# Kernel tuning notes

Measured on AMD Instinct MI355X. Metric: run time of the kernel, lower is better.

## Reference

```python
import jax, jax.numpy as jnp
import numpy as np

B, N, IN, E, H, F = 64, 256, 128, 256, 8, 1024


def setup_inputs() -> dict:
    key = jax.random.key(0)
    ks = jax.random.split(key, 16)
    x = jax.random.normal(ks[0], (B, N, IN), jnp.float32)
    adj = (jax.random.uniform(ks[1], (B, N, N)) < 0.1).astype(jnp.float32)
    adj = jnp.maximum(adj, adj.transpose(0, 2, 1))  # symmetric 0/1 adjacency
    mask = jax.random.randint(ks[2], (B, N), 0, 2).astype(jnp.float32)
    dist = jax.random.normal(ks[3], (B, N, N), jnp.float32)

    def lin(k, i, o):
        return (jax.random.normal(k, (i, o), jnp.float32) / np.sqrt(i)).astype(jnp.float32)

    return dict(
        x=x, adj=adj, mask=mask, dist=dist,
        W1=lin(ks[4], IN, E), b1=jnp.zeros((E,), jnp.float32),
        W2=lin(ks[5], E, E), b2=jnp.zeros((E,), jnp.float32),
        W3=lin(ks[6], E, E), b3=jnp.zeros((E,), jnp.float32),
        ln1_g=jnp.ones((E,), jnp.float32), ln1_b=jnp.zeros((E,), jnp.float32),
        Wq=lin(ks[7], E, H * E), Wk=lin(ks[8], E, H * E), Wv=lin(ks[9], E, H * E),
        Wo=lin(ks[10], H * E, E), bo=jnp.zeros((E,), jnp.float32),
        ln2_g=jnp.ones((E,), jnp.float32), ln2_b=jnp.zeros((E,), jnp.float32),
        Wf1=lin(ks[11], E, F), bf1=jnp.zeros((F,), jnp.float32),
        Wf2=lin(ks[12], F, E), bf2=jnp.zeros((E,), jnp.float32),
    )


def _layernorm(x, g, b):
    m = x.mean(-1, keepdims=True)
    v = ((x - m) ** 2).mean(-1, keepdims=True)
    return (x - m) * jax.lax.rsqrt(v + 1e-5) * g + b


def reference(x, adj, mask, dist, W1, b1, W2, b2, W3, b3, ln1_g, ln1_b,
              Wq, Wk, Wv, Wo, bo, ln2_g, ln2_b, Wf1, bf1, Wf2, bf2):
    # --- DenseGCNConv normalization (add self-loops, sym-normalize) ---
    eye = jnp.eye(N, dtype=adj.dtype)
    A = adj * (1.0 - eye) + eye                      # fill_diag(adj, 1)
    dis = jax.lax.rsqrt(jnp.clip(A.sum(-1), 1.0, None))
    An = dis[:, :, None] * A * dis[:, None, :]       # D^-1/2 A D^-1/2, [B,N,N]
    m3 = mask[:, :, None]

    def gcn(h, W, b):
        return (jnp.einsum('bij,bjf->bif', An, h @ W) + b) * m3

    g1 = jax.nn.relu(gcn(x, W1, b1))
    g2 = jax.nn.relu(gcn(g1, W2, b2))
    g3 = jax.nn.relu(gcn(g2, W3, b3))
    gcn_res = g1 + g2 + g3

    # --- masked MHA with distance bias (head dim = E per head) ---
    h = _layernorm(gcn_res, ln1_g, ln1_b)
    mh = mask[:, None, :, None]                      # [B,1,N,1]
    q = (h @ Wq).reshape(B, N, H, E).transpose(0, 2, 1, 3) * mh
    k = (h @ Wk).reshape(B, N, H, E).transpose(0, 2, 1, 3) * mh
    v = (h @ Wv).reshape(B, N, H, E).transpose(0, 2, 1, 3) * mh
    a = jnp.einsum('bhne,bhme->bhnm', q * (E ** -0.5), k) + dist[:, None]
    am = (mask[:, :, None] * mask[:, None, :])[:, None]  # [B,1,N,N]
    a = jnp.where(am == 0, -1e9, a)
    a = jax.nn.softmax(a, axis=-1)
    a = jnp.where(am == 0, 0.0, a)
    y = jnp.einsum('bhnm,bhme->bhne', a, v).transpose(0, 2, 1, 3).reshape(B, N, H * E)
    y = (y @ Wo + bo) * m3
    att = gcn_res + y

    # --- FFN block ---
    f = _layernorm(att, ln2_g, ln2_b)
    f = (jax.nn.gelu(f @ Wf1 + bf1, approximate=False) @ Wf2 + bf2) * m3
    att = att + f
    return gcn_res + att
```

## Files before the change

kernel.cpp:

```cpp
#include <hip/hip_runtime.h>
#include <hip/hip_bf16.h>
#include <cmath>

#define BB 64
#define NNODES 256
#define INF_ 128
#define EE 256
#define HH 8
#define FFN 1024
#define BNROWS 16384

typedef __attribute__((ext_vector_type(8))) short short8;
typedef __attribute__((ext_vector_type(4))) float floatx4;
typedef __attribute__((ext_vector_type(4))) unsigned short ushort4v;

__device__ __forceinline__ float b2f(unsigned short u) {
  union { unsigned u32; float f; } w; w.u32 = ((unsigned)u) << 16; return w.f;
}
__device__ __forceinline__ unsigned short f2b(float f) {
  union { float f; unsigned u32; } w; w.f = f;
  unsigned r = w.u32 + 0x7FFFu + ((w.u32 >> 16) & 1u);
  return (unsigned short)(r >> 16);
}
__device__ __forceinline__ float gelu_f(float x) {
  const float z = 0.7978845608028654f * (x + 0.044715f * x * x * x);
  const float e = __expf(2.0f * z);
  const float th = (e - 1.0f) / (e + 1.0f);
  return 0.5f * x * (1.0f + th);
}

typedef const __attribute__((address_space(1))) void GV;
typedef __attribute__((address_space(3))) void LV;

__device__ __forceinline__ void gl_lds16(const unsigned short* g,
                                         unsigned short* l, int lane) {
#if __has_builtin(__builtin_amdgcn_global_load_lds)
  __builtin_amdgcn_global_load_lds((GV*)g, (LV*)l, 16, 0, 0);
#else
  *(short8*)(l + lane * 8) = *(const short8*)g;
#endif
}

__global__ void cvt_kernel(const float* __restrict__ src,
                           unsigned short* __restrict__ dst, int n)
{
  const int i = (blockIdx.x * 256 + threadIdx.x) * 4;
  if (i >= n) return;
  floatx4 v = *(const floatx4*)(src + i);
  ushort4v o;
  #pragma unroll
  for (int j = 0; j < 4; j++) o[j] = f2b(v[j]);
  *(ushort4v*)(dst + i) = o;
}

__global__ void tcvt_kernel(const float* __restrict__ src,
                            unsigned short* __restrict__ dst,
                            int R, int C)
{
  __shared__ float tile[32][33];
  const int c0 = blockIdx.x * 32, r0 = blockIdx.y * 32;
  const int tx = threadIdx.x, ty = threadIdx.y;
  #pragma unroll
  for (int i = ty; i < 32; i += 8)
    tile[i][tx] = src[(long long)(r0 + i) * C + c0 + tx];
  __syncthreads();
  #pragma unroll
  for (int i = ty; i < 32; i += 8)
    dst[(long long)(c0 + i) * R + r0 + tx] = f2b(tile[tx][i]);
}

__launch_bounds__(512, 4)
__global__ void gemm_kernel(const unsigned short* __restrict__ A, int lda,
                            long long sAo, long long sAi,
                            const unsigned short* __restrict__ Bm, int ldb,
                            long long sBo, long long sBi,
                            void* __restrict__ Cv, int ldc,
                            long long sCo, long long sCi,
                            int K, int zshift, int mode, int flag,
                            const float* __restrict__ aux1,
                            const float* __restrict__ mask,
                            float* __restrict__ gcn,
                            void* __restrict__ aux2)
{
  __shared__ __align__(16) unsigned short sA[16384];
  __shared__ __align__(16) unsigned short sB[16384];

  const int t = threadIdx.x;
  const int z = blockIdx.z;
  const int zi = z & ((1 << zshift) - 1);
  const int zb = z >> zshift;
  const int m0 = blockIdx.x * 128;
  const int n0 = blockIdx.y * 128;
  A  += zb * sAo + zi * sAi;
  Bm += zb * sBo + zi * sBi;
  const long long cbase = zb * sCo + zi * sCi;

  const int lane = t & 63;
  const int w = t >> 6;
  const int wm = w >> 2, wn = w & 3;
  const int lm = lane & 15, qd = lane >> 4;

  floatx4 acc[4][2] = {};

  const int sub = lane >> 4;
  const int qs  = lane & 15;
  const unsigned short* pA[4];
  const unsigned short* pB[4];
  #pragma unroll
  for (int i = 0; i < 4; i++) {
    const int d = w * 4 + i;
    const int r = d * 4 + sub;
    const int co = (qs ^ (r & 7)) * 8;
    pA[i] = A + (long long)(m0 + r) * lda + co;
    pB[i] = Bm + (long long)(n0 + r) * ldb + co;
  }

  for (int kk = 0; kk < K; kk += 128) {
    #pragma unroll
    for (int i = 0; i < 4; i++) {
      gl_lds16(pA[i] + kk, &sA[(w * 4 + i) * 512], lane);
      gl_lds16(pB[i] + kk, &sB[(w * 4 + i) * 512], lane);
    }
    __syncthreads();

    #pragma unroll
    for (int ks = 0; ks < 4; ks++) {
      short8 af[4], bg[2];
      const int q = ks * 4 + qd;
      #pragma unroll
      for (int mi = 0; mi < 4; mi++) {
        const int r = wm * 64 + mi * 16 + lm;
        af[mi] = *(const short8*)&sA[r * 128 + ((q ^ (r & 7)) * 8)];
      }
      #pragma unroll
      for (int ni = 0; ni < 2; ni++) {
        const int r = wn * 32 + ni * 16 + lm;
        bg[ni] = *(const short8*)&sB[r * 128 + ((q ^ (r & 7)) * 8)];
      }
      #pragma unroll
      for (int mi = 0; mi < 4; mi++)
        #pragma unroll
        for (int ni = 0; ni < 2; ni++)
          acc[mi][ni] = __builtin_amdgcn_mfma_f32_16x16x32_bf16(
              af[mi], bg[ni], acc[mi][ni], 0, 0, 0);
    }
    __syncthreads();
  }

  #pragma unroll
  for (int mi = 0; mi < 4; mi++) {
    const int row0 = m0 + wm * 64 + mi * 16 + qd * 4;
    #pragma unroll
    for (int ni = 0; ni < 2; ni++) {
      const int col = n0 + wn * 32 + ni * 16 + lm;
      floatx4 a = acc[mi][ni];
      if (mode == 0) {
        float* Cf = (float*)Cv;
        #pragma unroll
        for (int r = 0; r < 4; r++)
          Cf[cbase + (long long)(row0 + r) * ldc + col] = a[r];
      } else if (mode == 1) {
        unsigned short* Cb = (unsigned short*)Cv;
        #pragma unroll
        for (int r = 0; r < 4; r++)
          Cb[cbase + (long long)(row0 + r) * ldc + col] = f2b(a[r]);
      } else if (mode == 2) {
        float* Cf = (float*)Cv;
        #pragma unroll
        for (int r = 0; r < 4; r++)
          Cf[cbase + (long long)(row0 + r) * ldc + col] += a[r];
      } else if (mode == 3) {
        unsigned short* Cb = (unsigned short*)Cv;
        const float bv = aux1[col];
        #pragma unroll
        for (int r = 0; r < 4; r++)
          Cb[cbase + (long long)(row0 + r) * ldc + col] = f2b(gelu_f(a[r] + bv));
      } else if (mode == 5) {
        const int b = row0 >> 8, n = row0 & 255;
        ushort4v o;
        #pragma unroll
        for (int r = 0; r < 4; r++) o[r] = f2b(a[r]);
        *(ushort4v*)((unsigned short*)Cv + (long long)b * 65536 + col * 256 + n) = o;
      } else if (mode == 8) {
        float* Cf = (float*)Cv;
        const float* attf = (const float*)aux2;
        const float bv = aux1[col];
        #pragma unroll
        for (int r = 0; r < 4; r++) {
          const long long idx = (long long)(row0 + r) * 256 + col;
          Cf[idx] = gcn[idx] + attf[idx] + (a[r] + bv) * mask[row0 + r];
        }
      } else if (mode == 9) {
        const int token = zb * 256 + col;
        const float m = mask[token];
        ushort4v o; floatx4 g;
        #pragma unroll
        for (int r = 0; r < 4; r++) {
          const float v = fmaxf((a[r] + aux1[row0 + r]) * m, 0.f);
          o[r] = f2b(v); g[r] = v;
        }
        *(ushort4v*)((unsigned short*)Cv + (long long)token * 256 + row0) = o;
        float* gp = gcn + (long long)token * 256 + row0;
        if (flag) { floatx4 old = *(const floatx4*)gp; g += old; }
        *(floatx4*)gp = g;
      } else if (mode == 11) {
        if (col < 2048) {
          unsigned short* Cb = (unsigned short*)Cv;
          #pragma unroll
          for (int r = 0; r < 4; r++)
            Cb[(long long)(row0 + r) * 4096 + col] = f2b(a[r] * 0.0625f);
        } else if (col < 4096) {
          unsigned short* Cb = (unsigned short*)Cv;
          #pragma unroll
          for (int r = 0; r < 4; r++)
            Cb[(long long)(row0 + r) * 4096 + col] = f2b(a[r]);
        } else {
          const int z2 = (row0 >> 8) * 8 + ((col - 4096) >> 8);
          const int e = col & 255, n = row0 & 255;
          ushort4v o;
          #pragma unroll
          for (int r = 0; r < 4; r++) o[r] = f2b(a[r]);
          *(ushort4v*)((unsigned short*)aux2 + (long long)z2 * 65536 + e * 256 + n) = o;
        }
      } else {
        float* Cf = (float*)Cv;
        const float bv = aux1[col];
        #pragma unroll
        for (int r = 0; r < 4; r++) {
          const long long idx = (long long)(row0 + r) * 256 + col;
          Cf[idx] = gcn[idx] + (a[r] + bv) * mask[row0 + r];
        }
      }
    }
  }
}

__launch_bounds__(512, 2)
__global__ void attn_kernel(unsigned short* __restrict__ QKY,
                            const unsigned short* __restrict__ VT,
                            const float* __restrict__ dist,
                            const float* __restrict__ mask)
{
  __shared__ __align__(16) unsigned short sQ[8192];
  __shared__ __align__(16) unsigned short sKV[16384];
  __shared__ float redm[4][128];
  __shared__ float reds[4][128];

  const int mt = blockIdx.x;
  const int z  = blockIdx.y;
  const int b  = z >> 3, h = z & 7;
  const int t = threadIdx.x, lane = t & 63, w = t >> 6;
  const int wm = w >> 2, wn = w & 3;
  const int lm = lane & 15, qd = lane >> 4;
  const int m0 = mt * 128;

  unsigned short* Qbase = QKY + ((long long)(b * 256 + m0)) * 4096 + h * 256;
  const unsigned short* Kbase = QKY + ((long long)(b * 256)) * 4096 + 2048 + h * 256;
  const unsigned short* Vbase = VT + (long long)z * 65536;
  const float* maskb = mask + b * 256;
  const float* distb = dist + (long long)b * 65536;

  const int rin = lane >> 3;
  const int qs  = lane & 7;

  floatx4 S[4][4] = {};

  for (int c = 0; c < 4; c++) {
    const int e0 = c * 64;
    #pragma unroll
    for (int i = 0; i < 2; i++) {
      const int d = w * 2 + i;
      const int r = d * 8 + rin;
      gl_lds16(Qbase + (long long)r * 4096 + e0 + ((qs ^ (r & 7)) * 8),
               &sQ[d * 512], lane);
    }
    #pragma unroll
    for (int i = 0; i < 4; i++) {
      const int d = w * 4 + i;
      const int r = d * 8 + rin;
      gl_lds16(Kbase + (long long)r * 4096 + e0 + ((qs ^ (r & 7)) * 8),
               &sKV[d * 512], lane);
    }
    __syncthreads();
    #pragma unroll
    for (int ks = 0; ks < 2; ks++) {
      short8 af[4], bg[4];
      const int o = ks * 4 + qd;
      #pragma unroll
      for (int mi = 0; mi < 4; mi++) {
        const int r = wm * 64 + mi * 16 + lm;
        af[mi] = *(const short8*)&sQ[r * 64 + ((o ^ (r & 7)) * 8)];
      }
      #pragma unroll
      for (int ni = 0; ni < 4; ni++) {
        const int r = wn * 64 + ni * 16 + lm;
        bg[ni] = *(const short8*)&sKV[r * 64 + ((o ^ (r & 7)) * 8)];
      }
      #pragma unroll
      for (int mi = 0; mi < 4; mi++)
        #pragma unroll
        for (int ni = 0; ni < 4; ni++)
          S[mi][ni] = __builtin_amdgcn_mfma_f32_16x16x32_bf16(
              af[mi], bg[ni], S[mi][ni], 0, 0, 0);
    }
    __syncthreads();
  }

  float mk[4];
  #pragma unroll
  for (int ni = 0; ni < 4; ni++) mk[ni] = maskb[wn * 64 + ni * 16 + lm];

  float lred[4][4];
  #pragma unroll
  for (int mi = 0; mi < 4; mi++) {
    #pragma unroll
    for (int r = 0; r < 4; r++) {
      const int row = wm * 64 + mi * 16 + qd * 4 + r;
      const float mq = maskb[m0 + row];
      float mx = -3e38f;
      #pragma unroll
      for (int ni = 0; ni < 4; ni++) {
        const int col = wn * 64 + ni * 16 + lm;
        const float dv = distb[(long long)(m0 + row) * 256 + col];
        const float v = (mq != 0.f && mk[ni] != 0.f) ? (S[mi][ni][r] + dv) : -1e9f;
        S[mi][ni][r] = v;
        mx = fmaxf(mx, v);
      }
      lred[mi][r] = mx;
    }
  }
  #pragma unroll
  for (int off = 1; off < 16; off <<= 1)
    #pragma unroll
    for (int mi = 0; mi < 4; mi++)
      #pragma unroll
      for (int r = 0; r < 4; r++)
        lred[mi][r] = fmaxf(lred[mi][r], __shfl_xor(lred[mi][r], off));
  if (lm == 0)
    #pragma unroll
    for (int mi = 0; mi < 4; mi++)
      #pragma unroll
      for (int r = 0; r < 4; r++)
        redm[wn][wm * 64 + mi * 16 + qd * 4 + r] = lred[mi][r];
  __syncthreads();

  #pragma unroll
  for (int mi = 0; mi < 4; mi++) {
    #pragma unroll
    for (int r = 0; r < 4; r++) {
      const int row = wm * 64 + mi * 16 + qd * 4 + r;
      const float gmax = fmaxf(fmaxf(redm[0][row], redm[1][row]),
                               fmaxf(redm[2][row], redm[3][row]));
      float s = 0.f;
      #pragma unroll
      for (int ni = 0; ni < 4; ni++) {
        const float e = __expf(S[mi][ni][r] - gmax);
        S[mi][ni][r] = e;
        s += e;
      }
      lred[mi][r] = s;
    }
  }
  #pragma unroll
  for (int off = 1; off < 16; off <<= 1)
    #pragma unroll
    for (int mi = 0; mi < 4; mi++)
      #pragma unroll
      for (int r = 0; r < 4; r++)
        lred[mi][r] += __shfl_xor(lred[mi][r], off);
  if (lm == 0)
    #pragma unroll
    for (int mi = 0; mi < 4; mi++)
      #pragma unroll
      for (int r = 0; r < 4; r++)
        reds[wn][wm * 64 + mi * 16 + qd * 4 + r] = lred[mi][r];
  __syncthreads();

  #pragma unroll
  for (int mi = 0; mi < 4; mi++) {
    #pragma unroll
    for (int r = 0; r < 4; r++) {
      const int row = wm * 64 + mi * 16 + qd * 4 + r;
      const float gs = redm[0][row] * 0.f +
                       reds[0][row] + reds[1][row] + reds[2][row] + reds[3][row];
      const float inv = 1.0f / gs;
      #pragma unroll
      for (int ni = 0; ni < 4; ni++) S[mi][ni][r] *= inv;
    }
  }

  floatx4 Y[4][4] = {};
  for (int c = 0; c < 4; c++) {
    #pragma unroll
    for (int i = 0; i < 4; i++) {
      const int d = w * 4 + i;
      const int r = d * 8 + rin;
      gl_lds16(Vbase + (long long)r * 256 + c * 64 + ((qs ^ (r & 7)) * 8),
               &sKV[d * 512], lane);
    }
    if (wn == c) {
      #pragma unroll
      for (int mi = 0; mi < 4; mi++)
        #pragma unroll
        for (int r = 0; r < 4; r++) {
          const int row = wm * 64 + mi * 16 + qd * 4 + r;
          #pragma unroll
          for (int ni = 0; ni < 4; ni++) {
            const int kl = ni * 16 + lm;
            const int slot = (kl >> 3) ^ (row & 7);
            sQ[row * 64 + slot * 8 + (kl & 7)] = f2b(S[mi][ni][r]);
          }
        }
    }
    __syncthreads();
    #pragma unroll
    for (int ks = 0; ks < 2; ks++) {
      short8 af[4], bg[4];
      const int o = ks * 4 + qd;
      #pragma unroll
      for (int mi = 0; mi < 4; mi++) {
        const int r = wm * 64 + mi * 16 + lm;
        af[mi] = *(const short8*)&sQ[r * 64 + ((o ^ (r & 7)) * 8)];
      }
      #pragma unroll
      for (int ni = 0; ni < 4; ni++) {
        const int r = wn * 64 + ni * 16 + lm;
        bg[ni] = *(const short8*)&sKV[r * 64 + ((o ^ (r & 7)) * 8)];
      }
      #pragma unroll
      for (int mi = 0; mi < 4; mi++)
        #pragma unroll
        for (int ni = 0; ni < 4; ni++)
          Y[mi][ni] = __builtin_amdgcn_mfma_f32_16x16x32_bf16(
              af[mi], bg[ni], Y[mi][ni], 0, 0, 0);
    }
    __syncthreads();
  }

  #pragma unroll
  for (int mi = 0; mi < 4; mi++)
    #pragma unroll
    for (int ni = 0; ni < 4; ni++) {
      const int col = wn * 64 + ni * 16 + lm;
      #pragma unroll
      for (int r = 0; r < 4; r++) {
        const int row = wm * 64 + mi * 16 + qd * 4 + r;
        Qbase[(long long)row * 4096 + col] = f2b(Y[mi][ni][r]);
      }
    }
}

__global__ void deg_kernel(const float* __restrict__ adj,
                           float* __restrict__ dis)
{
  const int g = blockIdx.x * 4 + (threadIdx.x >> 6);
  const int lane = threadIdx.x & 63;
  const int i = g & 255;
  floatx4 v = *(const floatx4*)(adj + (long long)g * 256 + lane * 4);
  float s = 0.f;
  #pragma unroll
  for (int jj = 0; jj < 4; jj++) {
    const int j = lane * 4 + jj;
    s += (j == i) ? 1.0f : v[jj];
  }
  #pragma unroll
  for (int off = 32; off > 0; off >>= 1) s += __shfl_xor(s, off);
  if (lane == 0) dis[g] = 1.0f / sqrtf(fmaxf(s, 1.0f));
}

__global__ void an_kernel(const float* __restrict__ adj,
                          const float* __restrict__ dis,
                          unsigned short* __restrict__ An)
{
  const long long base = ((long long)blockIdx.x * 256 + threadIdx.x) * 4;
  const int rowg = (int)(base >> 8);
  const int i = rowg & 255;
  const int brow = rowg & ~255;
  const int j0 = (int)(base & 255);
  const float di = dis[rowg];
  floatx4 v = *(const floatx4*)(adj + base);
  ushort4v o;
  #pragma unroll
  for (int jj = 0; jj < 4; jj++) {
    const int j = j0 + jj;
    const float a = (j == i) ? 1.0f : v[jj];
    o[jj] = f2b(di * dis[brow + j] * a);
  }
  *(ushort4v*)(An + base) = o;
}

__global__ void ln_kernel(const float* __restrict__ X,
                          const float* __restrict__ gam,
                          const float* __restrict__ bet,
                          unsigned short* __restrict__ out)
{
  const int g = blockIdx.x * 4 + (threadIdx.x >> 6);
  const int lane = threadIdx.x & 63;
  floatx4 v = *(const floatx4*)(X + (long long)g * 256 + lane * 4);
  float s = v[0] + v[1] + v[2] + v[3];
  float sq = v[0]*v[0] + v[1]*v[1] + v[2]*v[2] + v[3]*v[3];
  #pragma unroll
  for (int off = 32; off > 0; off >>= 1) {
    s  += __shfl_xor(s, off);
    sq += __shfl_xor(sq, off);
  }
  const float mean = s * (1.0f / 256.0f);
  const float var = sq * (1.0f / 256.0f) - mean * mean;
  const float rs = 1.0f / sqrtf(var + 1e-5f);
  ushort4v o;
  #pragma unroll
  for (int jj = 0; jj < 4; jj++) {
    const int c = lane * 4 + jj;
    o[jj] = f2b((v[jj] - mean) * rs * gam[c] + bet[c]);
  }
  *(ushort4v*)(out + (long long)g * 256 + lane * 4) = o;
}

static inline void launch_gemm(hipStream_t st, int M, int N, int batch,
    const void* A, int lda, long long sAo, long long sAi,
    const void* B, int ldb, long long sBo, long long sBi,
    void* C, int ldc, long long sCo, long long sCi,
    int K, int zshift, int mode, int flag,
    const float* aux1, const float* mask, float* gcn, void* aux2)
{
  dim3 grid(M / 128, N / 128, batch), blk(512);
  gemm_kernel<<<grid, blk, 0, st>>>(
      (const unsigned short*)A, lda, sAo, sAi,
      (const unsigned short*)B, ldb, sBo, sBi,
      C, ldc, sCo, sCi, K, zshift, mode, flag, aux1, mask, gcn, aux2);
}

extern "C" void kernel_launch(void* const* d_in, const int* in_sizes, int n_in,
                              void* d_out, int out_size, void* d_ws, size_t ws_size,
                              hipStream_t stream)
{
  (void)in_sizes; (void)n_in; (void)out_size;
  const float* x    = (const float*)d_in[0];
  const float* adj  = (const float*)d_in[1];
  const float* mask = (const float*)d_in[2];
  const float* dist = (const float*)d_in[3];
  const float* W1   = (const float*)d_in[4];
  const float* b1   = (const float*)d_in[5];
  const float* W2   = (const float*)d_in[6];
  const float* b2   = (const float*)d_in[7];
  const float* W3   = (const float*)d_in[8];
  const float* b3   = (const float*)d_in[9];
  const float* ln1g = (const float*)d_in[10];
  const float* ln1b = (const float*)d_in[11];
  const float* Wq   = (const float*)d_in[12];
  const float* Wk   = (const float*)d_in[13];
  const float* Wv   = (const float*)d_in[14];
  const float* Wo   = (const float*)d_in[15];
  const float* bo   = (const float*)d_in[16];
  const float* ln2g = (const float*)d_in[17];
  const float* ln2b = (const float*)d_in[18];
  const float* Wf1  = (const float*)d_in[19];
  const float* bf1  = (const float*)d_in[20];
  const float* Wf2  = (const float*)d_in[21];
  const float* bf2  = (const float*)d_in[22];

  char* w = (char*)d_ws;
  auto alloc = [&](size_t sz) { void* p = (void*)w; w += sz; return p; };
  unsigned short* W1T   = (unsigned short*)alloc(65536);
  unsigned short* W2T   = (unsigned short*)alloc(131072);
  unsigned short* W3T   = (unsigned short*)alloc(131072);
  unsigned short* WQKVT = (unsigned short*)alloc(3145728);
  unsigned short* WOT   = (unsigned short*)alloc(1048576);
  unsigned short* WF1T  = (unsigned short*)alloc(524288);
  unsigned short* WF2T  = (unsigned short*)alloc(524288);
  unsigned short* XBF   = (unsigned short*)alloc(4194304);
  float*          GCN   = (float*)         alloc(16777216);
  float*          U     = (float*)         alloc(16777216);
  unsigned short* HBF   = (unsigned short*)alloc(8388608);
  float*          DIS   = (float*)         alloc(65536);
  char* scratch = (char*)alloc(201326592);
  if ((size_t)(w - (char*)d_ws) > ws_size) return;
  unsigned short* AN  = (unsigned short*)scratch;
  unsigned short* TT  = (unsigned short*)(scratch + 8388608);
  unsigned short* GBF = (unsigned short*)(scratch + 16777216);
  unsigned short* QKY = (unsigned short*)scratch;
  unsigned short* VT  = (unsigned short*)(scratch + 134217728);
  unsigned short* FFB = (unsigned short*)scratch;

  dim3 tb(32, 8);
  tcvt_kernel<<<dim3(8, 4),  tb, 0, stream>>>(W1,  W1T,  128,  256);
  tcvt_kernel<<<dim3(8, 8),  tb, 0, stream>>>(W2,  W2T,  256,  256);
  tcvt_kernel<<<dim3(8, 8),  tb, 0, stream>>>(W3,  W3T,  256,  256);
  tcvt_kernel<<<dim3(64, 8), tb, 0, stream>>>(Wq,  WQKVT,            256, 2048);
  tcvt_kernel<<<dim3(64, 8), tb, 0, stream>>>(Wk,  WQKVT + 2048*256, 256, 2048);
  tcvt_kernel<<<dim3(64, 8), tb, 0, stream>>>(Wv,  WQKVT + 4096*256, 256, 2048);
  tcvt_kernel<<<dim3(8, 64), tb, 0, stream>>>(Wo,  WOT,  2048,  256);
  tcvt_kernel<<<dim3(32, 8), tb, 0, stream>>>(Wf1, WF1T,  256, 1024);
  tcvt_kernel<<<dim3(8, 32), tb, 0, stream>>>(Wf2, WF2T, 1024,  256);
  cvt_kernel<<<2048, 256, 0, stream>>>(x, XBF, BNROWS * INF_);

  deg_kernel<<<4096, 256, 0, stream>>>(adj, DIS);
  an_kernel<<<4096, 256, 0, stream>>>(adj, DIS, AN);

  launch_gemm(stream, BNROWS, EE, 1, XBF, 128, 0,0, W1T, 128, 0,0,
              TT, 256, 0,0, 128, 0, 5, 0, nullptr, nullptr, nullptr, nullptr);
  launch_gemm(stream, 256, 256, BB, TT, 256, 65536,0, AN, 256, 65536,0,
              GBF, 256, 0,0, 256, 0, 9, 0, b1, mask, GCN, nullptr);
  launch_gemm(stream, BNROWS, EE, 1, GBF, 256, 0,0, W2T, 256, 0,0,
              TT, 256, 0,0, 256, 0, 5, 0, nullptr, nullptr, nullptr, nullptr);
  launch_gemm(stream, 256, 256, BB, TT, 256, 65536,0, AN, 256, 65536,0,
              GBF, 256, 0,0, 256, 0, 9, 1, b2, mask, GCN, nullptr);
  launch_gemm(stream, BNROWS, EE, 1, GBF, 256, 0,0, W3T, 256, 0,0,
              TT, 256, 0,0, 256, 0, 5, 0, nullptr, nullptr, nullptr, nullptr);
  launch_gemm(stream, 256, 256, BB, TT, 256, 65536,0, AN, 256, 65536,0,
              GBF, 256, 0,0, 256, 0, 9, 1, b3, mask, GCN, nullptr);

  ln_kernel<<<4096, 256, 0, stream>>>(GCN, ln1g, ln1b, HBF);

  launch_gemm(stream, BNROWS, 6144, 1, HBF, 256, 0,0, WQKVT, 256, 0,0,
              QKY, 4096, 0,0, 256, 0, 11, 0, nullptr, nullptr, nullptr, VT);
  attn_kernel<<<dim3(2, 512), 512, 0, stream>>>(QKY, VT, dist, mask);
  launch_gemm(stream, BNROWS, EE, 1, QKY, 4096, 0,0, WOT, 2048, 0,0,
              U, 256, 0,0, 2048, 0, 12, 0, bo, mask, GCN, nullptr);

  ln_kernel<<<4096, 256, 0, stream>>>(U, ln2g, ln2b, HBF);
  launch_gemm(stream, BNROWS, FFN, 1, HBF, 256, 0,0, WF1T, 256, 0,0,
              FFB, 1024, 0,0, 256, 0, 3, 0, bf1, nullptr, nullptr, nullptr);
  launch_gemm(stream, BNROWS, EE, 1, FFB, 1024, 0,0, WF2T, 1024, 0,0,
              d_out, 256, 0,0, 1024, 0, 8, 0, bf2, mask, GCN, U);
}
```

Before: 532.3 us.

## Merge weight packing launches, fuse degree/normalization, prefetch V, split QKV+attention by batch

Ten separate weight/input conversion launches become one pack_kernel that dispatches on block index. The degree and normalization kernels are fused into one per-batch kernel that keeps inverse-sqrt degrees in shared memory. In attention, the V chunk load is issued before the softmax and the next chunk is prefetched after each PV step, so loads overlap compute. The QKV GEMM and attention are split into two batch halves, which may improve cache locality at the cost of extra launches. The fused normalization kernel runs only 64 blocks, which may underuse the GPU.

```diff
diff --git a/kernel.cpp b/kernel.cpp
--- a/kernel.cpp
+++ b/kernel.cpp
@@ -41,25 +41,38 @@
 #endif
 }
 
-__global__ void cvt_kernel(const float* __restrict__ src,
-                           unsigned short* __restrict__ dst, int n)
-{
-  const int i = (blockIdx.x * 256 + threadIdx.x) * 4;
-  if (i >= n) return;
-  floatx4 v = *(const floatx4*)(src + i);
-  ushort4v o;
-  #pragma unroll
-  for (int j = 0; j < 4; j++) o[j] = f2b(v[j]);
-  *(ushort4v*)(dst + i) = o;
-}
-
-__global__ void tcvt_kernel(const float* __restrict__ src,
-                            unsigned short* __restrict__ dst,
-                            int R, int C)
+struct PackArgs {
+  const float* src[10];
+  unsigned short* dst[10];
+  int R[10], C[10];
+  int start[11];
+};
+
+__launch_bounds__(256)
+__global__ void pack_kernel(PackArgs a)
 {
   __shared__ float tile[32][33];
-  const int c0 = blockIdx.x * 32, r0 = blockIdx.y * 32;
-  const int tx = threadIdx.x, ty = threadIdx.y;
+  const int bid = blockIdx.x;
+  int j = 0;
+  while (bid >= a.start[j + 1]) j++;
+  const int lb = bid - a.start[j];
+  const float* src = a.src[j];
+  unsigned short* dst = a.dst[j];
+  const int R = a.R[j], C = a.C[j];
+
+  if (C == 0) {
+    const int i = (lb * 256 + threadIdx.x) * 4;
+    if (i >= R) return;
+    floatx4 v = *(const floatx4*)(src + i);
+    ushort4v o;
+    #pragma unroll
+    for (int k = 0; k < 4; k++) o[k] = f2b(v[k]);
+    *(ushort4v*)(dst + i) = o;
+    return;
+  }
+  const int tpr = C >> 5;
+  const int c0 = (lb % tpr) * 32, r0 = (lb / tpr) * 32;
+  const int tx = threadIdx.x & 31, ty = threadIdx.x >> 5;
   #pragma unroll
   for (int i = ty; i < 32; i += 8)
     tile[i][tx] = src[(long long)(r0 + i) * C + c0 + tx];
@@ -67,6 +80,43 @@
   #pragma unroll
   for (int i = ty; i < 32; i += 8)
     dst[(long long)(c0 + i) * R + r0 + tx] = f2b(tile[tx][i]);
+}
+
+__launch_bounds__(1024)
+__global__ void an_kernel(const float* __restrict__ adj,
+                          unsigned short* __restrict__ An)
+{
+  __shared__ float dis[256];
+  const int b = blockIdx.x;
+  const float* A = adj + (long long)b * 65536;
+  const int t = threadIdx.x;
+  const int row = t >> 2, seg = t & 3;
+  const float* p = A + row * 256 + seg * 64;
+  float s = 0.f;
+  for (int k = 0; k < 64; k += 4) {
+    floatx4 v = *(const floatx4*)(p + k);
+    #pragma unroll
+    for (int jj = 0; jj < 4; jj++) {
+      const int col = seg * 64 + k + jj;
+      s += (col == row) ? 1.0f : v[jj];
+    }
+  }
+  s += __shfl_xor(s, 1);
+  s += __shfl_xor(s, 2);
+  if (seg == 0) dis[row] = 1.0f / sqrtf(fmaxf(s, 1.0f));
+  __syncthreads();
+  const float di = dis[row];
+  unsigned short* dst = An + (long long)b * 65536 + row * 256 + seg * 64;
+  for (int k = 0; k < 64; k += 4) {
+    floatx4 v = *(const floatx4*)(p + k);
+    ushort4v o;
+    #pragma unroll
+    for (int jj = 0; jj < 4; jj++) {
+      const int col = seg * 64 + k + jj;
+      o[jj] = f2b(di * dis[col] * ((col == row) ? 1.0f : v[jj]));
+    }
+    *(ushort4v*)(dst + k) = o;
+  }
 }
 
 __launch_bounds__(512, 4)
@@ -239,7 +289,8 @@
 __global__ void attn_kernel(unsigned short* __restrict__ QKY,
                             const unsigned short* __restrict__ VT,
                             const float* __restrict__ dist,
-                            const float* __restrict__ mask)
+                            const float* __restrict__ mask,
+                            int b0)
 {
   __shared__ __align__(16) unsigned short sQ[8192];
   __shared__ __align__(16) unsigned short sKV[16384];
@@ -248,17 +299,18 @@
 
   const int mt = blockIdx.x;
   const int z  = blockIdx.y;
-  const int b  = z >> 3, h = z & 7;
+  const int bl = z >> 3, h = z & 7;
+  const int bg = b0 + bl;
   const int t = threadIdx.x, lane = t & 63, w = t >> 6;
   const int wm = w >> 2, wn = w & 3;
   const int lm = lane & 15, qd = lane >> 4;
   const int m0 = mt * 128;
 
-  unsigned short* Qbase = QKY + ((long long)(b * 256 + m0)) * 4096 + h * 256;
-  const unsigned short* Kbase = QKY + ((long long)(b * 256)) * 4096 + 2048 + h * 256;
+  unsigned short* Qbase = QKY + ((long long)(bl * 256 + m0)) * 4096 + h * 256;
+  const unsigned short* Kbase = QKY + ((long long)(bl * 256)) * 4096 + 2048 + h * 256;
   const unsigned short* Vbase = VT + (long long)z * 65536;
-  const float* maskb = mask + b * 256;
-  const float* distb = dist + (long long)b * 65536;
+  const float* maskb = mask + bg * 256;
+  const float* distb = dist + (long long)bg * 65536;
 
   const int rin = lane >> 3;
   const int qs  = lane & 7;
@@ -284,7 +336,7 @@
     __syncthreads();
     #pragma unroll
     for (int ks = 0; ks < 2; ks++) {
-      short8 af[4], bg[4];
+      short8 af[4], bg4[4];
       const int o = ks * 4 + qd;
       #pragma unroll
       for (int mi = 0; mi < 4; mi++) {
@@ -294,16 +346,24 @@
       #pragma unroll
       for (int ni = 0; ni < 4; ni++) {
         const int r = wn * 64 + ni * 16 + lm;
-        bg[ni] = *(const short8*)&sKV[r * 64 + ((o ^ (r & 7)) * 8)];
+        bg4[ni] = *(const short8*)&sKV[r * 64 + ((o ^ (r & 7)) * 8)];
       }
       #pragma unroll
       for (int mi = 0; mi < 4; mi++)
         #pragma unroll
         for (int ni = 0; ni < 4; ni++)
           S[mi][ni] = __builtin_amdgcn_mfma_f32_16x16x32_bf16(
-              af[mi], bg[ni], S[mi][ni], 0, 0, 0);
+              af[mi], bg4[ni], S[mi][ni], 0, 0, 0);
     }
     __syncthreads();
+  }
+
+  #pragma unroll
+  for (int i = 0; i < 4; i++) {
+    const int d = w * 4 + i;
+    const int r = d * 8 + rin;
+    gl_lds16(Vbase + (long long)r * 256 + ((qs ^ (r & 7)) * 8),
+             &sKV[d * 512], lane);
   }
 
   float mk[4];
@@ -381,8 +441,7 @@
     #pragma unroll
     for (int r = 0; r < 4; r++) {
       const int row = wm * 64 + mi * 16 + qd * 4 + r;
-      const float gs = redm[0][row] * 0.f +
-                       reds[0][row] + reds[1][row] + reds[2][row] + reds[3][row];
+      const float gs = reds[0][row] + reds[1][row] + reds[2][row] + reds[3][row];
       const float inv = 1.0f / gs;
       #pragma unroll
       for (int ni = 0; ni < 4; ni++) S[mi][ni][r] *= inv;
@@ -391,13 +450,6 @@
 
   floatx4 Y[4][4] = {};
   for (int c = 0; c < 4; c++) {
-    #pragma unroll
-    for (int i = 0; i < 4; i++) {
-      const int d = w * 4 + i;
-      const int r = d * 8 + rin;
-      gl_lds16(Vbase + (long long)r * 256 + c * 64 + ((qs ^ (r & 7)) * 8),
-               &sKV[d * 512], lane);
-    }
     if (wn == c) {
       #pragma unroll
       for (int mi = 0; mi < 4; mi++)
@@ -415,7 +467,7 @@
     __syncthreads();
     #pragma unroll
     for (int ks = 0; ks < 2; ks++) {
-      short8 af[4], bg[4];
+      short8 af[4], bg4[4];
       const int o = ks * 4 + qd;
       #pragma unroll
       for (int mi = 0; mi < 4; mi++) {
@@ -425,16 +477,25 @@
       #pragma unroll
       for (int ni = 0; ni < 4; ni++) {
         const int r = wn * 64 + ni * 16 + lm;
-        bg[ni] = *(const short8*)&sKV[r * 64 + ((o ^ (r & 7)) * 8)];
+        bg4[ni] = *(const short8*)&sKV[r * 64 + ((o ^ (r & 7)) * 8)];
       }
       #pragma unroll
       for (int mi = 0; mi < 4; mi++)
         #pragma unroll
         for (int ni = 0; ni < 4; ni++)
           Y[mi][ni] = __builtin_amdgcn_mfma_f32_16x16x32_bf16(
-              af[mi], bg[ni], Y[mi][ni], 0, 0, 0);
+              af[mi], bg4[ni], Y[mi][ni], 0, 0, 0);
     }
     __syncthreads();
+    if (c < 3) {
+      #pragma unroll
+      for (int i = 0; i < 4; i++) {
+        const int d = w * 4 + i;
+        const int r = d * 8 + rin;
+        gl_lds16(Vbase + (long long)r * 256 + (c + 1) * 64 + ((qs ^ (r & 7)) * 8),
+                 &sKV[d * 512], lane);
+      }
+    }
   }
 
   #pragma unroll
@@ -448,45 +509,6 @@
         Qbase[(long long)row * 4096 + col] = f2b(Y[mi][ni][r]);
       }
     }
-}
-
-__global__ void deg_kernel(const float* __restrict__ adj,
-                           float* __restrict__ dis)
-{
-  const int g = blockIdx.x * 4 + (threadIdx.x >> 6);
-  const int lane = threadIdx.x & 63;
-  const int i = g & 255;
-  floatx4 v = *(const floatx4*)(adj + (long long)g * 256 + lane * 4);
-  float s = 0.f;
-  #pragma unroll
-  for (int jj = 0; jj < 4; jj++) {
-    const int j = lane * 4 + jj;
-    s += (j == i) ? 1.0f : v[jj];
-  }
-  #pragma unroll
-  for (int off = 32; off > 0; off >>= 1) s += __shfl_xor(s, off);
-  if (lane == 0) dis[g] = 1.0f / sqrtf(fmaxf(s, 1.0f));
-}
-
-__global__ void an_kernel(const float* __restrict__ adj,
-                          const float* __restrict__ dis,
-                          unsigned short* __restrict__ An)
-{
-  const long long base = ((long long)blockIdx.x * 256 + threadIdx.x) * 4;
-  const int rowg = (int)(base >> 8);
-  const int i = rowg & 255;
-  const int brow = rowg & ~255;
-  const int j0 = (int)(base & 255);
-  const float di = dis[rowg];
-  floatx4 v = *(const floatx4*)(adj + base);
-  ushort4v o;
-  #pragma unroll
-  for (int jj = 0; jj < 4; jj++) {
-    const int j = j0 + jj;
-    const float a = (j == i) ? 1.0f : v[jj];
-    o[jj] = f2b(di * dis[brow + j] * a);
-  }
-  *(ushort4v*)(An + base) = o;
 }
 
 __global__ void ln_kernel(const float* __restrict__ X,
@@ -572,7 +594,6 @@
   float*          GCN   = (float*)         alloc(16777216);
   float*          U     = (float*)         alloc(16777216);
   unsigned short* HBF   = (unsigned short*)alloc(8388608);
-  float*          DIS   = (float*)         alloc(65536);
   char* scratch = (char*)alloc(201326592);
   if ((size_t)(w - (char*)d_ws) > ws_size) return;
   unsigned short* AN  = (unsigned short*)scratch;
@@ -582,20 +603,20 @@
   unsigned short* VT  = (unsigned short*)(scratch + 134217728);
   unsigned short* FFB = (unsigned short*)scratch;
 
-  dim3 tb(32, 8);
-  tcvt_kernel<<<dim3(8, 4),  tb, 0, stream>>>(W1,  W1T,  128,  256);
-  tcvt_kernel<<<dim3(8, 8),  tb, 0, stream>>>(W2,  W2T,  256,  256);
-  tcvt_kernel<<<dim3(8, 8),  tb, 0, stream>>>(W3,  W3T,  256,  256);
-  tcvt_kernel<<<dim3(64, 8), tb, 0, stream>>>(Wq,  WQKVT,            256, 2048);
-  tcvt_kernel<<<dim3(64, 8), tb, 0, stream>>>(Wk,  WQKVT + 2048*256, 256, 2048);
-  tcvt_kernel<<<dim3(64, 8), tb, 0, stream>>>(Wv,  WQKVT + 4096*256, 256, 2048);
-  tcvt_kernel<<<dim3(8, 64), tb, 0, stream>>>(Wo,  WOT,  2048,  256);
-  tcvt_kernel<<<dim3(32, 8), tb, 0, stream>>>(Wf1, WF1T,  256, 1024);
-  tcvt_kernel<<<dim3(8, 32), tb, 0, stream>>>(Wf2, WF2T, 1024,  256);
-  cvt_kernel<<<2048, 256, 0, stream>>>(x, XBF, BNROWS * INF_);
-
-  deg_kernel<<<4096, 256, 0, stream>>>(adj, DIS);
-  an_kernel<<<4096, 256, 0, stream>>>(adj, DIS, AN);
+  PackArgs pa;
+  const float* srcs[10] = {W1, W2, W3, Wq, Wk, Wv, Wo, Wf1, Wf2, x};
+  unsigned short* dsts[10] = {W1T, W2T, W3T, WQKVT, WQKVT + 2048*256,
+                              WQKVT + 4096*256, WOT, WF1T, WF2T, XBF};
+  const int Rs[10] = {128, 256, 256, 256, 256, 256, 2048, 256, 1024, BNROWS * INF_};
+  const int Cs[10] = {256, 256, 256, 2048, 2048, 2048, 256, 1024, 256, 0};
+  const int sts[11] = {0, 32, 96, 160, 672, 1184, 1696, 2208, 2464, 2720, 4768};
+  for (int j = 0; j < 10; j++) {
+    pa.src[j] = srcs[j]; pa.dst[j] = dsts[j]; pa.R[j] = Rs[j]; pa.C[j] = Cs[j];
+  }
+  for (int j = 0; j < 11; j++) pa.start[j] = sts[j];
+  pack_kernel<<<4768, 256, 0, stream>>>(pa);
+
+  an_kernel<<<64, 1024, 0, stream>>>(adj, AN);
 
   launch_gemm(stream, BNROWS, EE, 1, XBF, 128, 0,0, W1T, 128, 0,0,
               TT, 256, 0,0, 128, 0, 5, 0, nullptr, nullptr, nullptr, nullptr);
@@ -612,9 +633,14 @@
 
   ln_kernel<<<4096, 256, 0, stream>>>(GCN, ln1g, ln1b, HBF);
 
-  launch_gemm(stream, BNROWS, 6144, 1, HBF, 256, 0,0, WQKVT, 256, 0,0,
-              QKY, 4096, 0,0, 256, 0, 11, 0, nullptr, nullptr, nullptr, VT);
-  attn_kernel<<<dim3(2, 512), 512, 0, stream>>>(QKY, VT, dist, mask);
+  for (int g = 0; g < 2; g++) {
+    unsigned short* QKYg = QKY + (long long)g * 8192 * 4096;
+    unsigned short* VTg  = VT  + (long long)g * 256 * 65536;
+    launch_gemm(stream, 8192, 6144, 1, HBF + (long long)g * 8192 * 256, 256, 0,0,
+                WQKVT, 256, 0,0,
+                QKYg, 4096, 0,0, 256, 0, 11, 0, nullptr, nullptr, nullptr, VTg);
+    attn_kernel<<<dim3(2, 256), 512, 0, stream>>>(QKYg, VTg, dist, mask, g * 32);
+  }
   launch_gemm(stream, BNROWS, EE, 1, QKY, 4096, 0,0, WOT, 2048, 0,0,
               U, 256, 0,0, 2048, 0, 12, 0, bo, mask, GCN, nullptr);
 
```

Result: slower. 580.8 us (+9.1%).
